# Performance work log

Hardware: AMD Instinct MI355X
Metric: run time of the kernel (lower is better)

Reference implementation:

```python
import jax, jax.numpy as jnp
import numpy as np

N = 8192
NUM_CLASSES = 5
DIM = 3
EPS = 15.0
MIN_POINTS = 5
N_BATCH = 2


def setup_inputs() -> dict:
    key = jax.random.key(0)
    k1, k2, k3, k4 = jax.random.split(key, 4)
    # coords in a 96^3 box so eps=15 neighborhoods contain > minPoints same-group points
    coords = jax.random.uniform(k1, (N, DIM)) * 96.0
    batch = jax.random.randint(k2, (N, 1), 0, N_BATCH).astype(jnp.float32)
    feat = jax.random.normal(k3, (N, 1))
    seg = jax.random.normal(k4, (N, NUM_CLASSES))
    x = jnp.concatenate([coords, batch, feat, seg], axis=1).astype(jnp.float32)
    return {"x": x}


def _dbscan_labels(x):
    """Per-point DBSCAN cluster labels, run independently per (batch, class) group.
    noise = -1; cluster ids start at 0 within each group, ordered by the smallest
    point index of each cluster's core component (matches the serial scan order
    of the original implementation). Border points get the smallest adjacent
    cluster id (= first cluster to reach them in the serial algorithm)."""
    data = x[:, :-NUM_CLASSES]                 # (N, dim+2)
    seg = x[:, -NUM_CLASSES:]                  # (N, C)
    cls = jnp.argmax(seg, axis=1).astype(jnp.int32)
    b = data[:, DIM].astype(jnp.int32)
    pts = data[:, :DIM]                        # (N, 3)
    group = b * NUM_CLASSES + cls              # (N,) group id per point

    # pairwise squared distances via gram trick; d < eps  <=>  d2 < eps^2
    p2 = jnp.sum(pts * pts, axis=1)
    d2 = p2[:, None] + p2[None, :] - 2.0 * (pts @ pts.T)
    same = group[:, None] == group[None, :]
    adj = same & (d2 < EPS * EPS)              # includes self (d2 ~ 0)
    core = jnp.sum(adj, axis=1) >= MIN_POINTS  # region_query counts self too
    adjcc = adj & core[:, None] & core[None, :]

    idx = jnp.arange(N, dtype=jnp.int32)
    SENT = jnp.int32(N)
    lab0 = jnp.where(core, idx, SENT)

    # connected components of core-core graph via min-label propagation + pointer jumping
    def cond(st):
        return st[1]

    def body(st):
        lab, _ = st
        m = jnp.min(jnp.where(adjcc, lab[None, :], SENT), axis=1)
        nl = jnp.minimum(lab, m)
        safe = jnp.where(core, nl, 0)          # nl < N for core points
        nl2 = jnp.where(core, jnp.minimum(nl, nl[safe]), SENT)
        return (nl2, jnp.any(nl2 != lab))

    rep, _ = jax.lax.while_loop(cond, body, (lab0, jnp.array(True)))

    # per-group sequential cluster ids, ordered by component representative index
    is_rep = core & (rep == idx)
    cid_of_rep = jnp.zeros((N,), jnp.int32)
    for g in range(N_BATCH * NUM_CLASSES):     # fixed small count of groups
        mg = is_rep & (group == g)
        cum = jnp.cumsum(mg.astype(jnp.int32))
        cid_of_rep = jnp.where(mg, cum - 1, cid_of_rep)
    core_cid = cid_of_rep[jnp.where(core, rep, 0)]

    # border points: min cluster id among adjacent core points (same group via adj)
    nb_core = adj & core[None, :]
    BIG = jnp.int32(2 ** 30)
    bcid = jnp.min(jnp.where(nb_core, core_cid[None, :], BIG), axis=1)
    has_core_nb = jnp.any(nb_core, axis=1)
    labels = jnp.where(core, core_cid, jnp.where(has_core_nb, bcid, -1))
    return labels


def reference(x):
    labels = _dbscan_labels(x)
    data = x[:, :-NUM_CLASSES]
    # fixed-shape equivalent of the cluster gather: clustered points keep their
    # data columns (the differentiable part of the original output), noise zeroed
    clustered = jnp.where(labels[:, None] >= 0, data, 0.0)
    return labels, clustered
```

## Files before the change

kernel.cpp:

```cpp
#include <hip/hip_runtime.h>
#include <cstdint>
#include <cstddef>

#define NPTS 8192
#define NWORDS 128
#define XCOLS 10
#define MIN_PTS 5
#define NGROUPS 10
#define BIGC 0x3fffffff

#define NLCAP 1536
#define NSLICE 24
#define ECAP_S 2048
#define EACAP 8192
#define PT 512
#define PWV 8
#define GT 1024
#define GWV 16
#define ROUNDS 16
#define FLAG_B 0x80000000u
#define FLAG_D 0x40000000u

__global__ void __launch_bounds__(PT) k_pairs(
        const float* __restrict__ x, unsigned int* __restrict__ eAll,
        int* __restrict__ ecnt, unsigned long long* __restrict__ corebm_g,
        int* __restrict__ nlist_g, int* __restrict__ nn_g) {
    __shared__ float4 pts[NLCAP];
    __shared__ unsigned long long masks[NWORDS];
    __shared__ int pref[NWORDS];
    __shared__ int srowdeg[64];
    __shared__ int scnt, nnS;

    const int g = blockIdx.x / NSLICE;
    const int s = blockIdx.x % NSLICE;
    const int tid = threadIdx.x, lane = tid & 63, wv = tid >> 6;

    for (int k = tid; k < NLCAP; k += PT)
        pts[k] = make_float4(0.f, 0.f, 0.f, 1.0e38f);
    if (tid < 64) srowdeg[tid] = 0;
    if (tid == 0) scnt = 0;

    for (int w = wv; w < NWORDS; w += PWV) {
        int i = w * 64 + lane;
        const float2* r2 = (const float2*)(x + (size_t)i * XCOLS);
        float2 c23 = r2[1];
        float2 c45 = r2[2];
        float2 c67 = r2[3];
        float2 c89 = r2[4];
        float best = c45.y; int bc = 0;
        if (c67.x > best) { best = c67.x; bc = 1; }
        if (c67.y > best) { best = c67.y; bc = 2; }
        if (c89.x > best) { best = c89.x; bc = 3; }
        if (c89.y > best) { best = c89.y; bc = 4; }
        unsigned long long bm = __ballot((int)c23.y * 5 + bc == g);
        if (lane == 0) masks[w] = bm;
    }
    __syncthreads();
    if (wv == 0) {
        int v0 = __popcll(masks[lane]);
        int incl = v0;
        #pragma unroll
        for (int st = 1; st < 64; st <<= 1) {
            int o = __shfl_up(incl, st);
            if (lane >= st) incl += o;
        }
        pref[lane] = incl - v0;
        int tot0 = __shfl(incl, 63);
        int v1 = __popcll(masks[64 + lane]);
        int incl1 = v1;
        #pragma unroll
        for (int st = 1; st < 64; st <<= 1) {
            int o = __shfl_up(incl1, st);
            if (lane >= st) incl1 += o;
        }
        pref[64 + lane] = tot0 + incl1 - v1;
        if (lane == 63) nnS = tot0 + incl1;
    }
    __syncthreads();
    for (int w = wv; w < NWORDS; w += PWV) {
        unsigned long long bm = masks[w];
        if ((bm >> lane) & 1ull) {
            int p = pref[w] + __popcll(bm & ((1ull << lane) - 1ull));
            if (p < NLCAP) {
                int i = w * 64 + lane;
                const float2* r2 = (const float2*)(x + (size_t)i * XCOLS);
                float2 c01 = r2[0]; float2 c23 = r2[1];
                float px = c01.x, py = c01.y, pz = c23.x;
                pts[p] = make_float4(px, py, pz,
                                     0.5f * (px*px + py*py + pz*pz) - 56.25f);
                if (s == 0) nlist_g[g * NLCAP + p] = i;
            }
        }
    }
    if (s == 0 && tid == 0) nn_g[g] = (nnS > NLCAP) ? NLCAP : nnS;
    __syncthreads();
    const int NN = (nnS > NLCAP) ? NLCAP : nnS;

    const int rrow = s + NSLICE * lane;
    const float4 qu = pts[rrow];
    int rdeg = 0;
    const int NC = (NN + 31) >> 5;
    unsigned int* eg = eAll + (size_t)(g * NSLICE + s) * ECAP_S;
    for (int c = wv; c < NC; c += PWV) {
        int base = c << 5;
        unsigned int bits = 0u;
        #pragma unroll
        for (int t = 0; t < 32; t++) {
            float4 qv = pts[base + t];
            float dt = qu.x*qv.x + qu.y*qv.y + qu.z*qv.z;
            bits |= (dt > qu.w + qv.w) ? (1u << t) : 0u;
        }
        rdeg += __popc(bits);
        int d = rrow - base;
        if (d >= 31) bits = 0u;
        else if (d >= 0) bits &= ~((2u << d) - 1u);
        int cnt = __popc(bits);
        int incl = cnt;
        #pragma unroll
        for (int st = 1; st < 64; st <<= 1) {
            int o = __shfl_up(incl, st);
            if (lane >= st) incl += o;
        }
        int tot = __shfl(incl, 63);
        if (tot > 0) {
            int rb = 0;
            if (lane == 63) rb = atomicAdd(&scnt, tot);
            rb = __shfl(rb, 63);
            unsigned int p = (unsigned int)(rb + incl - cnt);
            unsigned int b = bits;
            unsigned int uhi = (unsigned int)rrow << 11;
            while (b) {
                int t = __ffs(b) - 1; b &= b - 1;
                if (p < ECAP_S) eg[p] = uhi | (unsigned int)(base + t);
                p++;
            }
        }
    }
    if (rdeg > 0) atomicAdd(&srowdeg[lane], rdeg);
    __syncthreads();
    if (wv == 0) {
        unsigned long long cb = __ballot(srowdeg[lane] >= MIN_PTS);
        if (lane == 0) {
            corebm_g[g * NSLICE + s] = cb;
            ecnt[g * NSLICE + s] = (scnt > ECAP_S) ? ECAP_S : scnt;
        }
    }
}

__global__ void __launch_bounds__(GT) k_graph(
        const unsigned int* __restrict__ eAll, const int* __restrict__ ecnt,
        const unsigned long long* __restrict__ corebm_g,
        const int* __restrict__ nlist_g, const int* __restrict__ nn_g,
        const float* __restrict__ x, float* __restrict__ out) {
    __shared__ unsigned int eA[EACAP];
    __shared__ int spar[NLCAP];
    __shared__ int scid[NLCAP];
    __shared__ int sbmin[NLCAP];
    __shared__ int nlist[NLCAP];
    __shared__ unsigned long long cbm[NSLICE];
    __shared__ unsigned long long corelin[NLCAP/64];
    __shared__ unsigned long long repbm[NLCAP/64];
    __shared__ int pref24[NLCAP/64];
    __shared__ int offs[NSLICE], cnts[NSLICE];
    __shared__ int NAs;
    __shared__ int sflagA[ROUNDS];

    const int g = blockIdx.x;
    const int tid = threadIdx.x, lane = tid & 63, wv = tid >> 6;
    const int NN = nn_g[g];

    if (tid < ROUNDS) sflagA[tid] = 0;
    if (wv == 0) {
        int c = 0;
        if (lane < NSLICE) {
            c = ecnt[g * NSLICE + lane];
            c = (c > ECAP_S) ? ECAP_S : c;
            cbm[lane] = corebm_g[g * NSLICE + lane];
        }
        int incl = c;
        #pragma unroll
        for (int st = 1; st < 32; st <<= 1) {
            int o = __shfl_up(incl, st);
            if (lane >= st) incl += o;
        }
        if (lane < NSLICE) { offs[lane] = incl - c; cnts[lane] = c; }
        if (lane == NSLICE - 1) NAs = incl;
    }
    for (int k = tid; k < NLCAP; k += GT) {
        spar[k] = k;
        sbmin[k] = BIGC;
        nlist[k] = nlist_g[g * NLCAP + k];
    }
    __syncthreads();
    const int NA = (NAs > EACAP) ? EACAP : NAs;
    for (int s2 = wv; s2 < NSLICE; s2 += GWV) {
        const unsigned int* eg = eAll + (size_t)(g * NSLICE + s2) * ECAP_S;
        int off = offs[s2], cn = cnts[s2];
        for (int o = lane; o < cn; o += 64) {
            int dst = off + o;
            if (dst < EACAP) eA[dst] = eg[o];
        }
    }
    for (int w = wv; w < NLCAP / 64; w += GWV) {
        int l = w * 64 + lane;
        bool b = (cbm[l % NSLICE] >> (l / NSLICE)) & 1ull;
        unsigned long long bm = __ballot(b);
        if (lane == 0) corelin[w] = bm;
    }
    __syncthreads();
    auto corebit = [&](int l) -> bool { return (corelin[l >> 6] >> (l & 63)) & 1ull; };

    for (int r = 0; r < ROUNDS; r++) {
        for (int k = tid; k < NA; k += GT) {
            unsigned int pk = eA[k];
            if (pk & 0xC0000000u) continue;
            int u = (int)((pk >> 11) & 2047u), v = (int)(pk & 2047u);
            if (r == 0) {
                bool cu = corebit(u), cv = corebit(v);
                if (!(cu && cv)) {
                    eA[k] = pk | ((cu != cv) ? FLAG_B : FLAG_D);
                    continue;
                }
            }
            int ru = spar[u];
            while (true) { int p = spar[ru]; if (p == ru) break; ru = p; }
            int rv = spar[v];
            while (true) { int p = spar[rv]; if (p == rv) break; rv = p; }
            if (ru < rv)      { if (atomicMin(&spar[rv], ru) > ru) sflagA[r] = 1; }
            else if (rv < ru) { if (atomicMin(&spar[ru], rv) > rv) sflagA[r] = 1; }
        }
        __syncthreads();
        for (int k = tid; k < NN; k += GT) {
            int p = spar[k];
            while (true) { int q = spar[p]; if (q == p) break; p = q; }
            spar[k] = p;
        }
        __syncthreads();
        if (!sflagA[r]) break;
    }

    for (int w = wv; w < NLCAP / 64; w += GWV) {
        int l = w * 64 + lane;
        bool isr = (l < NN) && corebit(l) && (spar[l] == l);
        unsigned long long bm = __ballot(isr);
        if (lane == 0) repbm[w] = bm;
    }
    __syncthreads();
    if (wv == 0 && lane < NLCAP / 64) {
        int c = __popcll(repbm[lane]);
        int incl = c;
        #pragma unroll
        for (int st = 1; st < 32; st <<= 1) {
            int o = __shfl_up(incl, st);
            if (lane >= st) incl += o;
        }
        pref24[lane] = incl - c;
    }
    __syncthreads();
    for (int w = wv; w < NLCAP / 64; w += GWV) {
        int l = w * 64 + lane;
        unsigned long long bm = repbm[w];
        if ((bm >> lane) & 1ull)
            scid[l] = pref24[w] + __popcll(bm & ((1ull << lane) - 1ull));
    }
    __syncthreads();
    int cc[2];
    #pragma unroll
    for (int t = 0; t < 2; t++) {
        int k = tid + t * GT;
        cc[t] = (k < NN && corebit(k)) ? scid[spar[k]] : BIGC;
    }
    __syncthreads();
    #pragma unroll
    for (int t = 0; t < 2; t++) {
        int k = tid + t * GT;
        if (k < NLCAP) spar[k] = (k < NN) ? cc[t] : BIGC;
    }
    __syncthreads();
    for (int k = tid; k < NA; k += GT) {
        unsigned int pk = eA[k];
        if ((pk & 0xC0000000u) != FLAG_B) continue;
        int u = (int)((pk >> 11) & 2047u), v = (int)(pk & 2047u);
        int cu = spar[u], cv = spar[v];
        if (cu == BIGC) atomicMin(&sbmin[u], cv);
        else            atomicMin(&sbmin[v], cu);
    }
    __syncthreads();
    for (int k = tid; k < NN; k += GT) {
        int i = nlist[k];
        int c = spar[k];
        int lbl = (c != BIGC) ? c : ((sbmin[k] < BIGC) ? sbmin[k] : -1);
        out[i] = (float)lbl;
        const float* r = x + (size_t)i * XCOLS;
        float* o = out + NPTS + (size_t)i * 5;
        bool keep = lbl >= 0;
        #pragma unroll
        for (int c5 = 0; c5 < 5; c5++) o[c5] = keep ? r[c5] : 0.0f;
    }
}

extern "C" void kernel_launch(void* const* d_in, const int* in_sizes, int n_in,
                              void* d_out, int out_size, void* d_ws, size_t ws_size,
                              hipStream_t stream) {
    const float* x = (const float*)d_in[0];
    float* out = (float*)d_out;
    char* ws = (char*)d_ws;

    unsigned int* eAll       = (unsigned int*)(ws);
    int* ecnt                = (int*)(ws + 1966080);
    unsigned long long* cbm  = (unsigned long long*)(ws + 1967104);
    int* nlist_g             = (int*)(ws + 1969024);
    int* nn_g                = (int*)(ws + 2030464);

    k_pairs<<<NGROUPS * NSLICE, PT, 0, stream>>>(x, eAll, ecnt, cbm, nlist_g, nn_g);
    k_graph<<<NGROUPS, GT, 0, stream>>>(eAll, ecnt, cbm, nlist_g, nn_g, x, out);
}
```

Baseline: 88.58 us.

## Replace multi-round union-find with single-pass CAS union streaming edges from global

Replaces the iterative min-hooking connected-components loop, with its per-round barriers and path compression, by a single-pass lock-free union-find that links roots with atomicCAS and retries. Edges are now streamed straight from global memory in both the union and border passes, so the LDS edge buffer and its prefix-sum compaction are gone. The pair kernel's block size also grows from 512 to 1024 threads. The cost is reading edges from global twice and volatile LDS traversal that can contend under CAS retries.

```diff
diff --git a/kernel.cpp b/kernel.cpp
--- a/kernel.cpp
+++ b/kernel.cpp
@@ -12,14 +12,10 @@
 #define NLCAP 1536
 #define NSLICE 24
 #define ECAP_S 2048
-#define EACAP 8192
-#define PT 512
-#define PWV 8
+#define PT 1024
+#define PWV 16
 #define GT 1024
 #define GWV 16
-#define ROUNDS 16
-#define FLAG_B 0x80000000u
-#define FLAG_D 0x40000000u
 
 __global__ void __launch_bounds__(PT) k_pairs(
         const float* __restrict__ x, unsigned int* __restrict__ eAll,
@@ -152,39 +148,26 @@
         const unsigned long long* __restrict__ corebm_g,
         const int* __restrict__ nlist_g, const int* __restrict__ nn_g,
         const float* __restrict__ x, float* __restrict__ out) {
-    __shared__ unsigned int eA[EACAP];
     __shared__ int spar[NLCAP];
     __shared__ int scid[NLCAP];
+    __shared__ int scid2[NLCAP];
     __shared__ int sbmin[NLCAP];
     __shared__ int nlist[NLCAP];
     __shared__ unsigned long long cbm[NSLICE];
     __shared__ unsigned long long corelin[NLCAP/64];
     __shared__ unsigned long long repbm[NLCAP/64];
     __shared__ int pref24[NLCAP/64];
-    __shared__ int offs[NSLICE], cnts[NSLICE];
-    __shared__ int NAs;
-    __shared__ int sflagA[ROUNDS];
+    __shared__ int cnts[NSLICE];
 
     const int g = blockIdx.x;
     const int tid = threadIdx.x, lane = tid & 63, wv = tid >> 6;
     const int NN = nn_g[g];
-
-    if (tid < ROUNDS) sflagA[tid] = 0;
-    if (wv == 0) {
-        int c = 0;
-        if (lane < NSLICE) {
-            c = ecnt[g * NSLICE + lane];
-            c = (c > ECAP_S) ? ECAP_S : c;
-            cbm[lane] = corebm_g[g * NSLICE + lane];
-        }
-        int incl = c;
-        #pragma unroll
-        for (int st = 1; st < 32; st <<= 1) {
-            int o = __shfl_up(incl, st);
-            if (lane >= st) incl += o;
-        }
-        if (lane < NSLICE) { offs[lane] = incl - c; cnts[lane] = c; }
-        if (lane == NSLICE - 1) NAs = incl;
+    volatile int* vpar = spar;
+
+    if (wv == 0 && lane < NSLICE) {
+        int c = ecnt[g * NSLICE + lane];
+        cnts[lane] = (c > ECAP_S) ? ECAP_S : c;
+        cbm[lane] = corebm_g[g * NSLICE + lane];
     }
     for (int k = tid; k < NLCAP; k += GT) {
         spar[k] = k;
@@ -192,15 +175,6 @@
         nlist[k] = nlist_g[g * NLCAP + k];
     }
     __syncthreads();
-    const int NA = (NAs > EACAP) ? EACAP : NAs;
-    for (int s2 = wv; s2 < NSLICE; s2 += GWV) {
-        const unsigned int* eg = eAll + (size_t)(g * NSLICE + s2) * ECAP_S;
-        int off = offs[s2], cn = cnts[s2];
-        for (int o = lane; o < cn; o += 64) {
-            int dst = off + o;
-            if (dst < EACAP) eA[dst] = eg[o];
-        }
-    }
     for (int w = wv; w < NLCAP / 64; w += GWV) {
         int l = w * 64 + lane;
         bool b = (cbm[l % NSLICE] >> (l / NSLICE)) & 1ull;
@@ -210,35 +184,33 @@
     __syncthreads();
     auto corebit = [&](int l) -> bool { return (corelin[l >> 6] >> (l & 63)) & 1ull; };
 
-    for (int r = 0; r < ROUNDS; r++) {
-        for (int k = tid; k < NA; k += GT) {
-            unsigned int pk = eA[k];
-            if (pk & 0xC0000000u) continue;
-            int u = (int)((pk >> 11) & 2047u), v = (int)(pk & 2047u);
-            if (r == 0) {
-                bool cu = corebit(u), cv = corebit(v);
-                if (!(cu && cv)) {
-                    eA[k] = pk | ((cu != cv) ? FLAG_B : FLAG_D);
-                    continue;
-                }
+    for (int s2 = 0; s2 < NSLICE; s2++) {
+        int cn = cnts[s2];
+        const unsigned int* eg = eAll + (size_t)(g * NSLICE + s2) * ECAP_S;
+        for (int e = tid; e < cn; e += GT) {
+            unsigned int pk = eg[e];
+            int u = (int)(pk >> 11), v = (int)(pk & 2047u);
+            if (!(corebit(u) && corebit(v))) continue;
+            int ru = u;
+            while (true) { int p = vpar[ru]; if (p == ru) break; ru = p; }
+            int rv = v;
+            while (true) { int p = vpar[rv]; if (p == rv) break; rv = p; }
+            while (ru != rv) {
+                if (ru > rv) { int t = ru; ru = rv; rv = t; }
+                int old = atomicCAS(&spar[rv], rv, ru);
+                if (old == rv) break;
+                rv = old;
+                while (true) { int p = vpar[rv]; if (p == rv) break; rv = p; }
             }
-            int ru = spar[u];
-            while (true) { int p = spar[ru]; if (p == ru) break; ru = p; }
-            int rv = spar[v];
-            while (true) { int p = spar[rv]; if (p == rv) break; rv = p; }
-            if (ru < rv)      { if (atomicMin(&spar[rv], ru) > ru) sflagA[r] = 1; }
-            else if (rv < ru) { if (atomicMin(&spar[ru], rv) > rv) sflagA[r] = 1; }
-        }
-        __syncthreads();
-        for (int k = tid; k < NN; k += GT) {
-            int p = spar[k];
-            while (true) { int q = spar[p]; if (q == p) break; p = q; }
-            spar[k] = p;
-        }
-        __syncthreads();
-        if (!sflagA[r]) break;
-    }
-
+        }
+    }
+    __syncthreads();
+    for (int k = tid; k < NN; k += GT) {
+        int p = spar[k];
+        while (true) { int q = vpar[p]; if (q == p) break; p = q; }
+        spar[k] = p;
+    }
+    __syncthreads();
     for (int w = wv; w < NLCAP / 64; w += GWV) {
         int l = w * 64 + lane;
         bool isr = (l < NN) && corebit(l) && (spar[l] == l);
@@ -264,31 +236,25 @@
             scid[l] = pref24[w] + __popcll(bm & ((1ull << lane) - 1ull));
     }
     __syncthreads();
-    int cc[2];
-    #pragma unroll
-    for (int t = 0; t < 2; t++) {
-        int k = tid + t * GT;
-        cc[t] = (k < NN && corebit(k)) ? scid[spar[k]] : BIGC;
-    }
-    __syncthreads();
-    #pragma unroll
-    for (int t = 0; t < 2; t++) {
-        int k = tid + t * GT;
-        if (k < NLCAP) spar[k] = (k < NN) ? cc[t] : BIGC;
-    }
-    __syncthreads();
-    for (int k = tid; k < NA; k += GT) {
-        unsigned int pk = eA[k];
-        if ((pk & 0xC0000000u) != FLAG_B) continue;
-        int u = (int)((pk >> 11) & 2047u), v = (int)(pk & 2047u);
-        int cu = spar[u], cv = spar[v];
-        if (cu == BIGC) atomicMin(&sbmin[u], cv);
-        else            atomicMin(&sbmin[v], cu);
+    for (int k = tid; k < NLCAP; k += GT)
+        scid2[k] = (k < NN && corebit(k)) ? scid[spar[k]] : BIGC;
+    __syncthreads();
+    for (int s2 = 0; s2 < NSLICE; s2++) {
+        int cn = cnts[s2];
+        const unsigned int* eg = eAll + (size_t)(g * NSLICE + s2) * ECAP_S;
+        for (int e = tid; e < cn; e += GT) {
+            unsigned int pk = eg[e];
+            int u = (int)(pk >> 11), v = (int)(pk & 2047u);
+            bool cu = corebit(u), cv = corebit(v);
+            if (cu == cv) continue;
+            if (cu) atomicMin(&sbmin[v], scid2[u]);
+            else    atomicMin(&sbmin[u], scid2[v]);
+        }
     }
     __syncthreads();
     for (int k = tid; k < NN; k += GT) {
         int i = nlist[k];
-        int c = spar[k];
+        int c = scid2[k];
         int lbl = (c != BIGC) ? c : ((sbmin[k] < BIGC) ? sbmin[k] : -1);
         out[i] = (float)lbl;
         const float* r = x + (size_t)i * XCOLS;
```

After: 117.8 us. +33.0%, slower.
